# Kernel tuning notes

Measured on AMD Instinct MI355X. Metric: run time of the kernel, lower is better.

## Reference

```python
import jax, jax.numpy as jnp
import numpy as np

V, T, H, N, HID = 512, 64, 256, 1024, 100
D = V + T  # biLSTM input dim


def _lstm_dir(x, Wih, Whh, b, reverse):
    # x: [n, Din]; PyTorch gate order i,f,g,o; b = b_ih + b_hh (equivalent math)
    xw = x @ Wih.T + b  # [n, 4H] precomputed input projection
    if reverse:
        xw = xw[::-1]
    h_dim = Whh.shape[1]

    def step(carry, xt):
        h, c = carry
        g = xt + h @ Whh.T
        i, f, gg, o = jnp.split(g, 4, axis=-1)
        i = jax.nn.sigmoid(i)
        f = jax.nn.sigmoid(f)
        gg = jnp.tanh(gg)
        o = jax.nn.sigmoid(o)
        c = f * c + i * gg
        h = o * jnp.tanh(c)
        return (h, c), h

    init = (jnp.zeros((h_dim,), x.dtype), jnp.zeros((h_dim,), x.dtype))
    _, hs = jax.lax.scan(step, init, xw)
    return hs[::-1] if reverse else hs


def setup_inputs() -> dict:
    key = jax.random.key(0)
    ks = jax.random.split(key, 20)
    s = 1.0 / np.sqrt(H)  # PyTorch LSTM init scale
    inp = {
        "word_table": jax.random.normal(ks[0], (V, V), jnp.float32) * 0.1,
        "pos_table": jax.random.normal(ks[1], (T, T), jnp.float32) * 0.1,
        # layer 0 fwd/bwd
        "l0f_Wih": jax.random.uniform(ks[2], (4 * H, D), jnp.float32, -s, s),
        "l0f_Whh": jax.random.uniform(ks[3], (4 * H, H), jnp.float32, -s, s),
        "l0f_b": jax.random.uniform(ks[4], (4 * H,), jnp.float32, -s, s),
        "l0b_Wih": jax.random.uniform(ks[5], (4 * H, D), jnp.float32, -s, s),
        "l0b_Whh": jax.random.uniform(ks[6], (4 * H, H), jnp.float32, -s, s),
        "l0b_b": jax.random.uniform(ks[7], (4 * H,), jnp.float32, -s, s),
        # layer 1 fwd/bwd (input = 2H)
        "l1f_Wih": jax.random.uniform(ks[8], (4 * H, 2 * H), jnp.float32, -s, s),
        "l1f_Whh": jax.random.uniform(ks[9], (4 * H, H), jnp.float32, -s, s),
        "l1f_b": jax.random.uniform(ks[10], (4 * H,), jnp.float32, -s, s),
        "l1b_Wih": jax.random.uniform(ks[11], (4 * H, 2 * H), jnp.float32, -s, s),
        "l1b_Whh": jax.random.uniform(ks[12], (4 * H, H), jnp.float32, -s, s),
        "l1b_b": jax.random.uniform(ks[13], (4 * H,), jnp.float32, -s, s),
        # edge-scorer MLP: Linear(4H,100) -> tanh -> Linear(100,1)
        "mlp_W1": jax.random.uniform(ks[14], (HID, 4 * H), jnp.float32, -0.03, 0.03),
        "mlp_b1": jax.random.uniform(ks[15], (HID,), jnp.float32, -0.03, 0.03),
        "mlp_W2": jax.random.uniform(ks[16], (1, HID), jnp.float32, -0.1, 0.1),
        "mlp_b2": jax.random.uniform(ks[17], (1,), jnp.float32, -0.1, 0.1),
        "word_idx": jax.random.randint(ks[18], (1, N), 0, V),
        "pos_idx": jax.random.randint(ks[19], (1, N), 0, T),
    }
    return inp


def reference(word_table, pos_table,
              l0f_Wih, l0f_Whh, l0f_b, l0b_Wih, l0b_Whh, l0b_b,
              l1f_Wih, l1f_Whh, l1f_b, l1b_Wih, l1b_Whh, l1b_b,
              mlp_W1, mlp_b1, mlp_W2, mlp_b2,
              word_idx, pos_idx):
    # embedding lookups on external tables, cat word+pos -> [n, D]
    x = jnp.concatenate([word_table[word_idx[0]], pos_table[pos_idx[0]]], axis=-1)
    # 2-layer bidirectional LSTM, batch=1 (squeezed)
    h = jnp.concatenate([_lstm_dir(x, l0f_Wih, l0f_Whh, l0f_b, False),
                         _lstm_dir(x, l0b_Wih, l0b_Whh, l0b_b, True)], axis=-1)  # [n, 2H]
    h = jnp.concatenate([_lstm_dir(h, l1f_Wih, l1f_Whh, l1f_b, False),
                         _lstm_dir(h, l1b_Wih, l1b_Whh, l1b_b, True)], axis=-1)  # [n, 2H]
    # pairwise edge scorer: layer_2(tanh(layer_1(cat(h_head, h_mod))))
    # split W1 = [Wh | Wm] so the cat never materializes per pair
    two_h = h.shape[-1]
    Wh, Wm = mlp_W1[:, :two_h], mlp_W1[:, two_h:]
    A = h @ Wh.T  # [n, HID] head contribution
    B = h @ Wm.T  # [n, HID] modifier contribution
    hid = jnp.tanh(A[:, None, :] + B[None, :, :] + mlp_b1)  # [n, n, HID]
    scores = hid @ mlp_W2[0] + mlp_b2[0]  # [n, n]
    n = scores.shape[0]
    eye = jnp.eye(n, dtype=bool)
    scores = jnp.where(eye, 0.0, scores)  # diagonal left at 0, as in the torch loop
    return jax.nn.softmax(scores, axis=0)
```

## Files before the change

kernel.cpp:

```cpp
#include <hip/hip_runtime.h>
#include <hip/hip_bf16.h>


#define L2E 1.4426950408889634f

__device__ __forceinline__ float fast_rcp(float x) { return __builtin_amdgcn_rcpf(x); }
__device__ __forceinline__ float sigm_f(float x) {
    return fast_rcp(1.f + exp2f(-x * L2E));
}
__device__ __forceinline__ float tanh_f(float x) {
    return 1.f - 2.f * fast_rcp(1.f + exp2f(x * (2.f * L2E)));
}

__device__ __forceinline__ void st_msg(unsigned long long* p, unsigned long long m) {
    asm volatile("global_store_dwordx2 %0, %1, off sc0 sc1"
                 :: "v"(p), "v"(m) : "memory");
}

__device__ __forceinline__ unsigned long long poll_msg(
    const unsigned long long* p, unsigned want)
{
    unsigned long long r0, r1, r2, r3, r = 0;
    bool done = false;
    for (int it = 0; it < 4096 && !done; ++it) {
        asm volatile(
            "global_load_dwordx2 %0, %4, off sc0 sc1\n\t"
            "s_sleep 3\n\t"
            "global_load_dwordx2 %1, %4, off sc0 sc1\n\t"
            "s_sleep 3\n\t"
            "global_load_dwordx2 %2, %4, off sc0 sc1\n\t"
            "s_sleep 3\n\t"
            "global_load_dwordx2 %3, %4, off sc0 sc1\n\t"
            "s_waitcnt vmcnt(3)"
            : "=&v"(r0), "=&v"(r1), "=&v"(r2), "=&v"(r3)
            : "v"(p) : "memory");
        if (__all((unsigned)(r0 >> 32) == want)) { r = r0; done = true; }
        if (!done) {
            asm volatile("s_waitcnt vmcnt(2)" ::: "memory");
            if (__all((unsigned)(r1 >> 32) == want)) { r = r1; done = true; }
        }
        if (!done) {
            asm volatile("s_waitcnt vmcnt(1)" ::: "memory");
            if (__all((unsigned)(r2 >> 32) == want)) { r = r2; done = true; }
        }
        if (!done) {
            asm volatile("s_waitcnt vmcnt(0)" ::: "memory");
            if (__all((unsigned)(r3 >> 32) == want)) { r = r3; done = true; }
        }
        asm volatile("s_waitcnt vmcnt(0)" ::: "memory");
    }
    if (!done) {
        do {
            r = __hip_atomic_load(p, __ATOMIC_RELAXED, __HIP_MEMORY_SCOPE_AGENT);
        } while (!__all((unsigned)(r >> 32) == want));
    }
    return r;
}

__global__ __launch_bounds__(256) void embed_kernel(
    const float* __restrict__ wt, const float* __restrict__ pt,
    const int* __restrict__ wi, const int* __restrict__ pi,
    float* __restrict__ x)
{
    int idx = blockIdx.x * 256 + threadIdx.x;
    if (idx >= 1024 * 576) return;
    int n = idx / 576, c = idx % 576;
    x[idx] = (c < 512) ? wt[wi[n] * 512 + c] : pt[pi[n] * 64 + (c - 512)];
}

__global__ __launch_bounds__(256) void gemm_bias(
    const float* __restrict__ A,
    const float* __restrict__ W0, const float* __restrict__ W1,
    const float* __restrict__ b0, const float* __restrict__ b1,
    float* __restrict__ C0, float* __restrict__ C1,
    int M, int N, int K)
{
    const float* W = blockIdx.z ? W1 : W0;
    const float* bias = blockIdx.z ? b1 : b0;
    float* C = blockIdx.z ? C1 : C0;
    int m0 = blockIdx.y * 64, n0 = blockIdx.x * 64;
    __shared__ float As[16][65];
    __shared__ float Ws[16][65];
    int tid = threadIdx.x;
    int tx = tid & 15, ty = tid >> 4;
    float acc[4][4] = {};
    int lr = tid >> 2, lkc = (tid & 3) * 4;
    for (int k0 = 0; k0 < K; k0 += 16) {
        float4 a4 = *(const float4*)&A[(size_t)(m0 + lr) * K + k0 + lkc];
        float4 w4 = *(const float4*)&W[(size_t)(n0 + lr) * K + k0 + lkc];
        As[lkc + 0][lr] = a4.x; As[lkc + 1][lr] = a4.y;
        As[lkc + 2][lr] = a4.z; As[lkc + 3][lr] = a4.w;
        Ws[lkc + 0][lr] = w4.x; Ws[lkc + 1][lr] = w4.y;
        Ws[lkc + 2][lr] = w4.z; Ws[lkc + 3][lr] = w4.w;
        __syncthreads();
#pragma unroll
        for (int k = 0; k < 16; k++) {
            float a[4], b[4];
#pragma unroll
            for (int i = 0; i < 4; i++) a[i] = As[k][ty * 4 + i];
#pragma unroll
            for (int j = 0; j < 4; j++) b[j] = Ws[k][tx * 4 + j];
#pragma unroll
            for (int i = 0; i < 4; i++)
#pragma unroll
                for (int j = 0; j < 4; j++) acc[i][j] += a[i] * b[j];
        }
        __syncthreads();
    }
    int colbase = n0 + tx * 4;
    float4 bv = *(const float4*)&bias[colbase];
#pragma unroll
    for (int i = 0; i < 4; i++) {
        float4 o;
        o.x = acc[i][0] + bv.x; o.y = acc[i][1] + bv.y;
        o.z = acc[i][2] + bv.z; o.w = acc[i][3] + bv.w;
        *(float4*)&C[(size_t)(m0 + ty * 4 + i) * N + colbase] = o;
    }
}

__global__ __launch_bounds__(512, 2) void lstm_scan(
    const float* __restrict__ xw_f, const float* __restrict__ xw_b,
    const float* __restrict__ Whh_f, const float* __restrict__ Whh_b,
    float* __restrict__ hout,
    unsigned long long* __restrict__ hx)
{
    const int sub  = blockIdx.x;
    const int tid  = threadIdx.x;
    const int lane = tid & 63;
    const int wv   = tid >> 6;
    const int dsel = tid >> 8;
    const int tl   = tid & 255;
    const int kh   = tl >> 7;
    const int lrow = tl & 127;
    const int R    = (lrow >> 5) * 256 + sub * 32 + (lrow & 31);

    const float* __restrict__ xw  = dsel ? xw_b : xw_f;
    const float* __restrict__ Whh = dsel ? Whh_b : Whh_f;
    const float4* __restrict__ Wr =
        (const float4*)(Whh + (size_t)R * 256 + (kh << 7));

    __shared__ float h0_sh[256], h1_sh[256];
    __shared__ float part0[256], part1[256];
    float* __restrict__ h_sh  = dsel ? h1_sh : h0_sh;
    float* __restrict__ partd = dsel ? part1 : part0;

    const bool isProd = (wv == 0 || wv == 4) && lane < 32;
    float c = 0.f;
    if (tid < 256) { h0_sh[tid] = 0.f; h1_sh[tid] = 0.f; }
    __syncthreads();

    for (int t = 0; t < 1024; t++) {
        const int trow = dsel ? (1023 - t) : t;

        float xg0 = 0.f, xg1 = 0.f, xg2 = 0.f, xg3 = 0.f;
        if (isProd) {
            const float* xr = &xw[(size_t)trow * 1024 + sub * 32 + lane];
            xg0 = xr[0];   xg1 = xr[256];
            xg2 = xr[512]; xg3 = xr[768];
        }

        float a0 = 0.f, a1 = 0.f, a2 = 0.f, a3 = 0.f;
        const float4* hp4 = (const float4*)&h_sh[kh << 7];
#pragma unroll
        for (int i = 0; i < 16; i += 4) {
            float4 h0v = hp4[i + 0], w0v = Wr[i + 0];
            float4 h1v = hp4[i + 1], w1v = Wr[i + 1];
            float4 h2v = hp4[i + 2], w2v = Wr[i + 2];
            float4 h3v = hp4[i + 3], w3v = Wr[i + 3];
            a0 += w0v.x * h0v.x + w0v.y * h0v.y + w0v.z * h0v.z + w0v.w * h0v.w;
            a1 += w1v.x * h1v.x + w1v.y * h1v.y + w1v.z * h1v.z + w1v.w * h1v.w;
            a2 += w2v.x * h2v.x + w2v.y * h2v.y + w2v.z * h2v.z + w2v.w * h2v.w;
            a3 += w3v.x * h3v.x + w3v.y * h3v.y + w3v.z * h3v.z + w3v.w * h3v.w;
        }
        partd[tl] = (a0 + a1) + (a2 + a3);
        __syncthreads();

        const int par = (t + 1) & 1;
        if (isProd) {
            float s0 = partd[lane]      + partd[128 + lane]  + xg0;
            float s1 = partd[32 + lane] + partd[160 + lane]  + xg1;
            float s2 = partd[64 + lane] + partd[192 + lane]  + xg2;
            float s3 = partd[96 + lane] + partd[224 + lane]  + xg3;
            float iv = sigm_f(s0), fv = sigm_f(s1);
            float gv = tanh_f(s2), ov = sigm_f(s3);
            c = fv * c + iv * gv;
            float h = ov * tanh_f(c);
            if (t + 1 < 1024) {
                unsigned long long msg =
                    ((unsigned long long)(unsigned)(t + 1) << 32) |
                    (unsigned long long)__float_as_uint(h);
                st_msg(&hx[(((sub << 1) + par) << 6) + (dsel << 5) + lane], msg);
                h_sh[sub * 32 + lane] = h;
            }
            hout[(size_t)trow * 512 + (dsel << 8) + sub * 32 + lane] = h;
        }
        if (wv != 0 && t + 1 < 1024) {
            int pw = (sub + wv) & 7;
            const unsigned long long* sp =
                &hx[(((pw << 1) + par) << 6) + lane];
            unsigned long long v = poll_msg(sp, (unsigned)(t + 1));
            float hv = __uint_as_float((unsigned)v);
            ((lane < 32) ? h0_sh : h1_sh)[pw * 32 + (lane & 31)] = hv;
        }
        __syncthreads();
    }
}

__global__ __launch_bounds__(256) void transpose_w1(
    const float* __restrict__ W1, float* __restrict__ W1T)
{
    int idx = blockIdx.x * 256 + threadIdx.x;
    if (idx >= 100 * 1024) return;
    int n = idx / 1024, j = idx % 1024;
    W1T[j * 100 + n] = W1[idx];
}

__global__ __launch_bounds__(256) void ab_kernel(
    const float* __restrict__ h1, const float* __restrict__ W1T,
    const float* __restrict__ b1v,
    float* __restrict__ Ab, float* __restrict__ Bb)
{
    int m0 = blockIdx.x * 16;
    __shared__ float hs[16][512];
    int tid = threadIdx.x;
    for (int idx = tid * 4; idx < 16 * 512; idx += 1024) {
        int r = idx >> 9, cc = idx & 511;
        *(float4*)&hs[r][cc] = *(const float4*)&h1[(size_t)(m0 + r) * 512 + cc];
    }
    __syncthreads();
    bool isB = tid >= 128;
    int n = tid & 127;
    if (n < 100) {
        float acc[16] = {};
        const float* wbase = W1T + (isB ? 512 * 100 : 0) + n;
#pragma unroll 4
        for (int k = 0; k < 512; k++) {
            float wv = wbase[k * 100];
#pragma unroll
            for (int m = 0; m < 16; m++) acc[m] += hs[m][k] * wv;
        }
        float badd = isB ? 0.f : b1v[n];
        float* dst = isB ? Bb : Ab;
#pragma unroll
        for (int m = 0; m < 16; m++) dst[(m0 + m) * 100 + n] = acc[m] + badd;
    }
}

__global__ __launch_bounds__(256) void pair_kernel(
    const float* __restrict__ Ab, const float* __restrict__ Bb,
    const float* __restrict__ W2, const float* __restrict__ b2,
    float* __restrict__ sT)
{
    int i0 = blockIdx.x * 32, j0 = blockIdx.y * 32;
    __shared__ float Ash[32][101];
    __shared__ float Bsh[32][101];
    __shared__ float w2s[100];
    int tid = threadIdx.x;
    for (int idx = tid; idx < 3200; idx += 256) {
        int r = idx / 100, cc = idx % 100;
        Ash[r][cc] = Ab[(i0 + r) * 100 + cc];
        Bsh[r][cc] = Bb[(j0 + r) * 100 + cc];
    }
    if (tid < 100) w2s[tid] = W2[tid];
    __syncthreads();
    float b2v = b2[0];
    int il = (tid & 15) * 2, jl = (tid >> 4) * 2;
    float a00 = 0.f, a01 = 0.f, a10 = 0.f, a11 = 0.f;
#pragma unroll 4
    for (int k = 0; k < 100; k++) {
        float wv = w2s[k];
        float x0 = Ash[il][k], x1 = Ash[il + 1][k];
        float y0 = Bsh[jl][k], y1 = Bsh[jl + 1][k];
        a00 += wv * tanh_f(x0 + y0);
        a01 += wv * tanh_f(x0 + y1);
        a10 += wv * tanh_f(x1 + y0);
        a11 += wv * tanh_f(x1 + y1);
    }
    float vals[2][2] = {{a00, a01}, {a10, a11}};
#pragma unroll
    for (int a = 0; a < 2; a++)
#pragma unroll
        for (int b = 0; b < 2; b++) {
            int gi2 = i0 + il + a, gj = j0 + jl + b;
            float v = vals[a][b] + b2v;
            if (gi2 == gj) v = 0.f;
            sT[(size_t)gj * 1024 + gi2] = v;
        }
}

__global__ __launch_bounds__(256) void colstats(
    const float* __restrict__ sT, float* __restrict__ mx, float* __restrict__ rs)
{
    int j = blockIdx.x;
    const float* row = sT + (size_t)j * 1024;
    int tid = threadIdx.x;
    __shared__ float red[256];
    float m = -INFINITY;
    for (int i = tid; i < 1024; i += 256) m = fmaxf(m, row[i]);
    red[tid] = m; __syncthreads();
    for (int s = 128; s > 0; s >>= 1) {
        if (tid < s) red[tid] = fmaxf(red[tid], red[tid + s]);
        __syncthreads();
    }
    float mxv = red[0];
    __syncthreads();
    float ssum = 0.f;
    for (int i = tid; i < 1024; i += 256) ssum += exp2f((row[i] - mxv) * L2E);
    red[tid] = ssum; __syncthreads();
    for (int s = 128; s > 0; s >>= 1) {
        if (tid < s) red[tid] += red[tid + s];
        __syncthreads();
    }
    if (tid == 0) { mx[j] = mxv; rs[j] = 1.f / red[0]; }
}

__global__ __launch_bounds__(256) void writeout(
    const float* __restrict__ sT, const float* __restrict__ mx,
    const float* __restrict__ rs, float* __restrict__ out)
{
    int i0 = blockIdx.x * 32, j0 = blockIdx.y * 32;
    __shared__ float til[32][33];
    int tid = threadIdx.x;
    int r = tid >> 3, c4 = (tid & 7) * 4;
    float4 v = *(const float4*)&sT[(size_t)(j0 + r) * 1024 + i0 + c4];
    til[r][c4 + 0] = v.x; til[r][c4 + 1] = v.y;
    til[r][c4 + 2] = v.z; til[r][c4 + 3] = v.w;
    __syncthreads();
    float4 o;
    float* op = &out[(size_t)(i0 + r) * 1024 + j0 + c4];
    o.x = exp2f((til[c4 + 0][r] - mx[j0 + c4 + 0]) * L2E) * rs[j0 + c4 + 0];
    o.y = exp2f((til[c4 + 1][r] - mx[j0 + c4 + 1]) * L2E) * rs[j0 + c4 + 1];
    o.z = exp2f((til[c4 + 2][r] - mx[j0 + c4 + 2]) * L2E) * rs[j0 + c4 + 2];
    o.w = exp2f((til[c4 + 3][r] - mx[j0 + c4 + 3]) * L2E) * rs[j0 + c4 + 3];
    *(float4*)op = o;
}

extern "C" void kernel_launch(void* const* d_in, const int* in_sizes, int n_in,
                              void* d_out, int out_size, void* d_ws, size_t ws_size,
                              hipStream_t stream)
{
    const float* word_table = (const float*)d_in[0];
    const float* pos_table  = (const float*)d_in[1];
    const float* l0f_Wih = (const float*)d_in[2];
    const float* l0f_Whh = (const float*)d_in[3];
    const float* l0f_b   = (const float*)d_in[4];
    const float* l0b_Wih = (const float*)d_in[5];
    const float* l0b_Whh = (const float*)d_in[6];
    const float* l0b_b   = (const float*)d_in[7];
    const float* l1f_Wih = (const float*)d_in[8];
    const float* l1f_Whh = (const float*)d_in[9];
    const float* l1f_b   = (const float*)d_in[10];
    const float* l1b_Wih = (const float*)d_in[11];
    const float* l1b_Whh = (const float*)d_in[12];
    const float* l1b_b   = (const float*)d_in[13];
    const float* mlp_W1  = (const float*)d_in[14];
    const float* mlp_b1  = (const float*)d_in[15];
    const float* mlp_W2  = (const float*)d_in[16];
    const float* mlp_b2  = (const float*)d_in[17];
    const int*   word_idx = (const int*)d_in[18];
    const int*   pos_idx  = (const int*)d_in[19];
    float* out = (float*)d_out;

    float* ws = (float*)d_ws;
    const size_t OFF_X   = 0;
    const size_t OFF_XWF = 589824;
    const size_t OFF_XWB = 1638400;
    const size_t OFF_H0  = 2686976;
    const size_t OFF_H1  = 3211264;
    const size_t OFF_W1T = 3735552;
    const size_t OFF_A   = 3837952;
    const size_t OFF_B   = 3940352;
    const size_t OFF_ST  = 4042752;
    const size_t OFF_MX  = 5091328;
    const size_t OFF_RS  = 5092352;
    const size_t OFF_HX  = 5095424;

    float* x   = ws + OFF_X;
    float* xwf = ws + OFF_XWF;
    float* xwb = ws + OFF_XWB;
    float* h0  = ws + OFF_H0;
    float* h1  = ws + OFF_H1;
    float* w1t = ws + OFF_W1T;
    float* Ab  = ws + OFF_A;
    float* Bb  = ws + OFF_B;
    float* sT  = ws + OFF_ST;
    float* mx  = ws + OFF_MX;
    float* rs  = ws + OFF_RS;
    unsigned long long* hx0 = (unsigned long long*)(ws + OFF_HX);
    unsigned long long* hx1 = hx0 + 1024;

    hipMemsetAsync(hx0, 0, 2048 * sizeof(unsigned long long), stream);

    embed_kernel<<<(1024 * 576 + 255) / 256, 256, 0, stream>>>(
        word_table, pos_table, word_idx, pos_idx, x);

    transpose_w1<<<(100 * 1024 + 255) / 256, 256, 0, stream>>>(mlp_W1, w1t);

    gemm_bias<<<dim3(16, 16, 2), 256, 0, stream>>>(
        x, l0f_Wih, l0b_Wih, l0f_b, l0b_b, xwf, xwb, 1024, 1024, 576);

    lstm_scan<<<8, 512, 0, stream>>>(
        xwf, xwb, l0f_Whh, l0b_Whh, h0, hx0);

    gemm_bias<<<dim3(16, 16, 2), 256, 0, stream>>>(
        h0, l1f_Wih, l1b_Wih, l1f_b, l1b_b, xwf, xwb, 1024, 1024, 512);

    lstm_scan<<<8, 512, 0, stream>>>(
        xwf, xwb, l1f_Whh, l1b_Whh, h1, hx1);

    ab_kernel<<<64, 256, 0, stream>>>(h1, w1t, mlp_b1, Ab, Bb);

    pair_kernel<<<dim3(32, 32), 256, 0, stream>>>(Ab, Bb, mlp_W2, mlp_b2, sT);

    colstats<<<1024, 256, 0, stream>>>(sT, mx, rs);

    writeout<<<dim3(32, 32), 256, 0, stream>>>(sT, mx, rs, out);
}
```

Baseline: 4.097 ms.

## Split LSTM scan over 16 blocks with register-resident recurrent weights

Result: faster. 3.718 ms, median of 2 (-9.2%).

```diff
diff --git a/kernel.cpp b/kernel.cpp
--- a/kernel.cpp
+++ b/kernel.cpp
@@ -22,14 +22,11 @@
 {
     unsigned long long r0, r1, r2, r3, r = 0;
     bool done = false;
-    for (int it = 0; it < 4096 && !done; ++it) {
+    for (int it = 0; it < 8192 && !done; ++it) {
         asm volatile(
             "global_load_dwordx2 %0, %4, off sc0 sc1\n\t"
-            "s_sleep 3\n\t"
             "global_load_dwordx2 %1, %4, off sc0 sc1\n\t"
-            "s_sleep 3\n\t"
             "global_load_dwordx2 %2, %4, off sc0 sc1\n\t"
-            "s_sleep 3\n\t"
             "global_load_dwordx2 %3, %4, off sc0 sc1\n\t"
             "s_waitcnt vmcnt(3)"
             : "=&v"(r0), "=&v"(r1), "=&v"(r2), "=&v"(r3)
@@ -130,57 +127,62 @@
     const int wv   = tid >> 6;
     const int dsel = tid >> 8;
     const int tl   = tid & 255;
-    const int kh   = tl >> 7;
-    const int lrow = tl & 127;
-    const int R    = (lrow >> 5) * 256 + sub * 32 + (lrow & 31);
-
-    const float* __restrict__ xw  = dsel ? xw_b : xw_f;
+    const int q    = tl >> 6;
+    const int lr   = tl & 63;
+    const int R    = (lr >> 4) * 256 + sub * 16 + (lr & 15);
+
     const float* __restrict__ Whh = dsel ? Whh_b : Whh_f;
-    const float4* __restrict__ Wr =
-        (const float4*)(Whh + (size_t)R * 256 + (kh << 7));
+
+    float4 w4[16];
+    {
+        const float4* Wr = (const float4*)(Whh + (size_t)R * 256 + (q << 6));
+#pragma unroll
+        for (int i = 0; i < 16; i++) w4[i] = Wr[i];
+    }
 
     __shared__ float h0_sh[256], h1_sh[256];
     __shared__ float part0[256], part1[256];
-    float* __restrict__ h_sh  = dsel ? h1_sh : h0_sh;
+    float* __restrict__ h_shd = dsel ? h1_sh : h0_sh;
     float* __restrict__ partd = dsel ? part1 : part0;
 
-    const bool isProd = (wv == 0 || wv == 4) && lane < 32;
+    const bool isProd = (wv == 0) && (lane < 32);
     float c = 0.f;
     if (tid < 256) { h0_sh[tid] = 0.f; h1_sh[tid] = 0.f; }
     __syncthreads();
 
     for (int t = 0; t < 1024; t++) {
-        const int trow = dsel ? (1023 - t) : t;
-
         float xg0 = 0.f, xg1 = 0.f, xg2 = 0.f, xg3 = 0.f;
         if (isProd) {
-            const float* xr = &xw[(size_t)trow * 1024 + sub * 32 + lane];
+            int pd = lane >> 4, hid = lane & 15;
+            int trp = pd ? (1023 - t) : t;
+            const float* xr = (pd ? xw_b : xw_f) +
+                              (size_t)trp * 1024 + sub * 16 + hid;
             xg0 = xr[0];   xg1 = xr[256];
             xg2 = xr[512]; xg3 = xr[768];
         }
 
         float a0 = 0.f, a1 = 0.f, a2 = 0.f, a3 = 0.f;
-        const float4* hp4 = (const float4*)&h_sh[kh << 7];
+        const float4* hp4 = (const float4*)&h_shd[q << 6];
 #pragma unroll
         for (int i = 0; i < 16; i += 4) {
-            float4 h0v = hp4[i + 0], w0v = Wr[i + 0];
-            float4 h1v = hp4[i + 1], w1v = Wr[i + 1];
-            float4 h2v = hp4[i + 2], w2v = Wr[i + 2];
-            float4 h3v = hp4[i + 3], w3v = Wr[i + 3];
-            a0 += w0v.x * h0v.x + w0v.y * h0v.y + w0v.z * h0v.z + w0v.w * h0v.w;
-            a1 += w1v.x * h1v.x + w1v.y * h1v.y + w1v.z * h1v.z + w1v.w * h1v.w;
-            a2 += w2v.x * h2v.x + w2v.y * h2v.y + w2v.z * h2v.z + w2v.w * h2v.w;
-            a3 += w3v.x * h3v.x + w3v.y * h3v.y + w3v.z * h3v.z + w3v.w * h3v.w;
+            float4 h0v = hp4[i + 0], h1v = hp4[i + 1];
+            float4 h2v = hp4[i + 2], h3v = hp4[i + 3];
+            a0 += w4[i+0].x*h0v.x + w4[i+0].y*h0v.y + w4[i+0].z*h0v.z + w4[i+0].w*h0v.w;
+            a1 += w4[i+1].x*h1v.x + w4[i+1].y*h1v.y + w4[i+1].z*h1v.z + w4[i+1].w*h1v.w;
+            a2 += w4[i+2].x*h2v.x + w4[i+2].y*h2v.y + w4[i+2].z*h2v.z + w4[i+2].w*h2v.w;
+            a3 += w4[i+3].x*h3v.x + w4[i+3].y*h3v.y + w4[i+3].z*h3v.z + w4[i+3].w*h3v.w;
         }
         partd[tl] = (a0 + a1) + (a2 + a3);
         __syncthreads();
 
         const int par = (t + 1) & 1;
         if (isProd) {
-            float s0 = partd[lane]      + partd[128 + lane]  + xg0;
-            float s1 = partd[32 + lane] + partd[160 + lane]  + xg1;
-            float s2 = partd[64 + lane] + partd[192 + lane]  + xg2;
-            float s3 = partd[96 + lane] + partd[224 + lane]  + xg3;
+            int pd = lane >> 4, hid = lane & 15;
+            const float* pp = pd ? part1 : part0;
+            float s0 = pp[hid]       + pp[64 + hid]  + pp[128 + hid]  + pp[192 + hid]  + xg0;
+            float s1 = pp[16 + hid]  + pp[80 + hid]  + pp[144 + hid]  + pp[208 + hid]  + xg1;
+            float s2 = pp[32 + hid]  + pp[96 + hid]  + pp[160 + hid]  + pp[224 + hid]  + xg2;
+            float s3 = pp[48 + hid]  + pp[112 + hid] + pp[176 + hid]  + pp[240 + hid]  + xg3;
             float iv = sigm_f(s0), fv = sigm_f(s1);
             float gv = tanh_f(s2), ov = sigm_f(s3);
             c = fv * c + iv * gv;
@@ -189,20 +191,29 @@
                 unsigned long long msg =
                     ((unsigned long long)(unsigned)(t + 1) << 32) |
                     (unsigned long long)__float_as_uint(h);
-                st_msg(&hx[(((sub << 1) + par) << 6) + (dsel << 5) + lane], msg);
-                h_sh[sub * 32 + lane] = h;
+                st_msg(&hx[(((sub << 1) + par) << 5) + lane], msg);
+                (pd ? h1_sh : h0_sh)[sub * 16 + hid] = h;
             }
-            hout[(size_t)trow * 512 + (dsel << 8) + sub * 32 + lane] = h;
-        }
-        if (wv != 0 && t + 1 < 1024) {
-            int pw = (sub + wv) & 7;
+            int trp = pd ? (1023 - t) : t;
+            hout[(size_t)trp * 512 + (pd << 8) + sub * 16 + hid] = h;
+        }
+        if (t + 1 < 1024 && (wv != 0 || lane >= 32)) {
+            int pw = (wv == 0) ? ((sub + 8) & 15)
+                               : ((lane < 32) ? ((sub + wv) & 15)
+                                              : ((sub + wv + 8) & 15));
             const unsigned long long* sp =
-                &hx[(((pw << 1) + par) << 6) + lane];
+                &hx[(((pw << 1) + par) << 5) + (lane & 31)];
             unsigned long long v = poll_msg(sp, (unsigned)(t + 1));
             float hv = __uint_as_float((unsigned)v);
-            ((lane < 32) ? h0_sh : h1_sh)[pw * 32 + (lane & 31)] = hv;
-        }
-        __syncthreads();
+            int hl = lane & 31;
+            ((hl < 16) ? h0_sh : h1_sh)[pw * 16 + (hl & 15)] = hv;
+        }
+        __syncthreads();
+
+#pragma unroll
+        for (int i = 0; i < 16; i++)
+            asm volatile("" : "+v"(w4[i].x), "+v"(w4[i].y),
+                              "+v"(w4[i].z), "+v"(w4[i].w));
     }
 }
 
@@ -399,13 +410,13 @@
     gemm_bias<<<dim3(16, 16, 2), 256, 0, stream>>>(
         x, l0f_Wih, l0b_Wih, l0f_b, l0b_b, xwf, xwb, 1024, 1024, 576);
 
-    lstm_scan<<<8, 512, 0, stream>>>(
+    lstm_scan<<<16, 512, 0, stream>>>(
         xwf, xwb, l0f_Whh, l0b_Whh, h0, hx0);
 
     gemm_bias<<<dim3(16, 16, 2), 256, 0, stream>>>(
         h0, l1f_Wih, l1b_Wih, l1f_b, l1b_b, xwf, xwb, 1024, 1024, 512);
 
-    lstm_scan<<<8, 512, 0, stream>>>(
+    lstm_scan<<<16, 512, 0, stream>>>(
         xwf, xwb, l1f_Whh, l1b_Whh, h1, hx1);
 
     ab_kernel<<<64, 256, 0, stream>>>(h1, w1t, mlp_b1, Ab, Bb);
```
